# Optimization experiments

Hardware: AMD Instinct MI355X
Metric: run time of the kernel (lower is better)

## Reference

```python
import jax, jax.numpy as jnp
import numpy as np
import math

B, T = 32, 64
VOCAB = 50005
EMB = 512
HID = 1024
SES = 1024
KNOW = 8785
NEG = math.exp(-100)

def _glorot(key, shape):
    fan_in, fan_out = shape[1], shape[0]
    lim = (6.0 / (fan_in + fan_out)) ** 0.5
    return jax.random.uniform(key, shape, jnp.float32, -lim, lim)

def setup_inputs() -> dict:
    key = jax.random.key(0)
    ks = jax.random.split(key, 16)
    inp = {}
    inp['ses_encoding'] = jax.random.normal(ks[0], (B, 1, SES), jnp.float32)
    inp['know_encoding'] = jax.random.normal(ks[1], (B, 1, SES), jnp.float32)
    inp['target'] = jax.random.randint(ks[2], (B, T), 0, 50000)
    inp['embed_w'] = jax.random.normal(ks[3], (VOCAB, EMB), jnp.float32) * 0.02
    # GRU params (PyTorch layout: W_ih [3H, E], W_hh [3H, H], gate order r,z,n)
    s = 1.0 / (HID ** 0.5)
    inp['W_ih'] = jax.random.uniform(ks[4], (3 * HID, EMB), jnp.float32, -s, s)
    inp['W_hh'] = jax.random.uniform(ks[5], (3 * HID, HID), jnp.float32, -s, s)
    inp['b_ih'] = jax.random.uniform(ks[6], (3 * HID,), jnp.float32, -s, s)
    inp['b_hh'] = jax.random.uniform(ks[7], (3 * HID,), jnp.float32, -s, s)
    inp['ses_to_dec_w'] = _glorot(ks[8], (HID, SES))
    inp['ses_to_dec_b'] = jnp.zeros((HID,), jnp.float32)
    inp['dec_inf_w'] = _glorot(ks[9], (2 * EMB, HID))
    inp['ses_inf_w'] = _glorot(ks[10], (2 * EMB, SES))
    inp['emb_inf_w'] = _glorot(ks[11], (2 * EMB, EMB))
    inp['emb_inf_b'] = jnp.zeros((2 * EMB,), jnp.float32)
    inp['W1'] = jax.random.normal(ks[12], (VOCAB, SES), jnp.float32) * 0.02
    inp['W2'] = jax.random.normal(ks[13], (VOCAB, SES), jnp.float32) * 0.02
    inp['W3'] = jax.random.normal(ks[14], (VOCAB, 2 * EMB), jnp.float32) * 0.02
    inp['W4'] = jax.random.normal(ks[15], (VOCAB, EMB), jnp.float32) * 0.02
    inp['know_vote_w'] = _glorot(jax.random.fold_in(key, 99), (KNOW, SES))
    return inp

def _gru_step(x, h, W_ih, W_hh, b_ih, b_hh):
    # x: [B,E], h: [B,H]
    gi = x @ W_ih.T + b_ih
    gh = h @ W_hh.T + b_hh
    ir, iz, inn = jnp.split(gi, 3, axis=-1)
    hr, hz, hn = jnp.split(gh, 3, axis=-1)
    r = jax.nn.sigmoid(ir + hr)
    z = jax.nn.sigmoid(iz + hz)
    n = jnp.tanh(inn + r * hn)
    return (1.0 - z) * h + z * n  # torch: h' = (1-z)*n + z*h with torch z; note torch formula

def _gru_step_torch(x, h, W_ih, W_hh, b_ih, b_hh):
    gi = x @ W_ih.T + b_ih
    gh = h @ W_hh.T + b_hh
    ir, iz, inn = jnp.split(gi, 3, axis=-1)
    hr, hz, hn = jnp.split(gh, 3, axis=-1)
    r = jax.nn.sigmoid(ir + hr)
    z = jax.nn.sigmoid(iz + hz)
    n = jnp.tanh(inn + r * hn)
    return (1.0 - z) * n + z * h

def reference(ses_encoding, know_encoding, target, embed_w, W_ih, W_hh, b_ih, b_hh,
              ses_to_dec_w, ses_to_dec_b, dec_inf_w, ses_inf_w, emb_inf_w, emb_inf_b,
              W1, W2, W3, W4, know_vote_w):
    ses = ses_encoding[:, 0, :]    # [B, SES]
    know = know_encoding[:, 0, :]  # [B, SES]
    target_emb = embed_w[target]   # [B, T, E]

    h0 = jnp.tanh(ses @ ses_to_dec_w.T + ses_to_dec_b)  # [B, H]

    # time-invariant pieces
    ses_inf_vec = ses @ ses_inf_w.T                      # [B, 2E]
    l1 = ses @ W1.T                                      # [B, V]
    l2 = know @ W2.T                                     # [B, V]
    # knowledge mixture log-probs (constant over time)
    ks = know @ know_vote_w.T                            # [B, KNOW]
    ks = ks[:, :-1]                                      # drop last -> [B, KNOW-1]
    pad_l = jnp.full((ks.shape[0], 10), NEG, ks.dtype)
    pad_r = jnp.full((ks.shape[0], VOCAB - 10 - (KNOW - 1)), NEG, ks.dtype)
    know_scores = jnp.concatenate([pad_l, ks, pad_r], axis=1)  # [B, V]
    know_probs = jax.nn.log_softmax(know_scores, axis=-1)      # [B, V]
    gate_const = l1 + l2                                 # [B, V]

    def step(h, emb_t):
        # emb_t: [B, E]
        h_new = _gru_step_torch(emb_t, h, W_ih, W_hh, b_ih, b_hh)  # [B, H]
        dec_hid_vec = h_new @ dec_inf_w.T                          # [B, 2E]
        target_inf = emb_t @ emb_inf_w.T + emb_inf_b               # [B, 2E]
        total = dec_hid_vec + ses_inf_vec + target_inf             # [B, 2E]
        mx = jnp.max(total.reshape(total.shape[0], EMB, 2), axis=-1)  # maxout -> [B, E]
        logits = mx @ embed_w.T                                    # shared embedding -> [B, V]
        hid_probs = jax.nn.log_softmax(logits, axis=-1)
        l3 = h_new @ W3.T                                          # note: W3 applied to hid_o [B,H]... but W3 is [V,2E]
        l4 = emb_t @ W4.T                                          # [B, V]
        gate = jax.nn.sigmoid(gate_const + l3 + l4)                # [B, V]
        final = gate * hid_probs + (1.0 - gate) * know_probs       # [B, V]
        return h_new, final

    # target_emb time-major for scan
    _, outs = jax.lax.scan(step, h0, jnp.swapaxes(target_emb, 0, 1))
    final_scores_all = jnp.swapaxes(outs, 0, 1)  # [B, T, V]
    return final_scores_all
```

## Files before the change

kernel.cpp:

```cpp
#include <hip/hip_runtime.h>

constexpr int VOC  = 50005;
constexpr int VOCP = 50048;
constexpr int NTM  = 391;
constexpr int NTMP = 400;
constexpr int KSN  = 8784;
constexpr int KSNP = 8832;
constexpr float NPAD = 41221.0f;

typedef unsigned short u16;
typedef __attribute__((ext_vector_type(4))) float f32x4;
typedef __attribute__((ext_vector_type(8))) short bf16x8;

__device__ __forceinline__ float dot4(float4 a, float4 b) {
    return a.x*b.x + a.y*b.y + a.z*b.z + a.w*b.w;
}
__device__ __forceinline__ float sigmoidf_(float x) { return 1.0f / (1.0f + expf(-x)); }
__device__ __forceinline__ u16 f2bf(float f) {
    unsigned x = __float_as_uint(f);
    return (u16)((x + 0x7FFFu + ((x >> 16) & 1u)) >> 16);
}
__device__ __forceinline__ float bf2f(u16 u) { return __uint_as_float(((unsigned)u) << 16); }
template<int AUX>
__device__ __forceinline__ void gload_lds16x(const void* g, void* l) {
    __builtin_amdgcn_global_load_lds((const __attribute__((address_space(1))) unsigned int*)g,
                                     (__attribute__((address_space(3))) unsigned int*)l, 16, 0, AUX);
}
__device__ __forceinline__ void gload_lds16(const void* g, void* l) { gload_lds16x<0>(g, l); }
__device__ __forceinline__ void store_u16_sc(u16* p, u16 v) {
    asm volatile("global_store_short %0, %1, off sc0 sc1" :: "v"(p), "v"((unsigned)v) : "memory");
}

__global__ __launch_bounds__(256) void k_cvt(const float* __restrict__ src, u16* __restrict__ dst,
                                             int ncols, int sld, int dld) {
    int row = blockIdx.x;
    int c = (blockIdx.y * 256 + threadIdx.x) * 4;
    if (c >= ncols) return;
    float4 v = *(const float4*)(src + (size_t)row * sld + c);
    unsigned lo = f2bf(v.x) | ((unsigned)f2bf(v.y) << 16);
    unsigned hi = f2bf(v.z) | ((unsigned)f2bf(v.w) << 16);
    *(uint2*)(dst + (size_t)row * dld + c) = make_uint2(lo, hi);
}

__global__ __launch_bounds__(256) void k_pad0(u16* __restrict__ Aemb, u16* __restrict__ A34,
                                              u16* __restrict__ Awk) {
    int r = VOC + blockIdx.x;
    unsigned* pe = (unsigned*)(Aemb + (size_t)r * 512);
    if (threadIdx.x < 256) pe[threadIdx.x] = 0;
    unsigned* p3 = (unsigned*)(A34 + (size_t)r * 1536);
    for (int i = threadIdx.x; i < 768; i += 256) p3[i] = 0;
    unsigned* pw = (unsigned*)(Awk + (size_t)r * 2048);
    for (int i = threadIdx.x; i < 1024; i += 256) pw[i] = 0;
}
__global__ __launch_bounds__(256) void k_padK(u16* __restrict__ kvwb) {
    int r = KSN + blockIdx.x;
    unsigned* p = (unsigned*)(kvwb + (size_t)r * 1024);
    for (int i = threadIdx.x; i < 512; i += 256) p[i] = 0;
}

__global__ __launch_bounds__(256) void k_bsk(const float* __restrict__ ses,
                                             const float* __restrict__ know,
                                             u16* __restrict__ Bsk) {
    int row = blockIdx.x;
    for (int c0 = threadIdx.x * 4; c0 < 2048; c0 += 1024) {
        uint2 val = make_uint2(0, 0);
        if (row < 32) {
            const float* srcp = (c0 < 1024) ? ses + (size_t)row * 1024 + c0
                                            : know + (size_t)row * 1024 + (c0 - 1024);
            float4 v = *(const float4*)srcp;
            val = make_uint2(f2bf(v.x) | ((unsigned)f2bf(v.y) << 16),
                             f2bf(v.z) | ((unsigned)f2bf(v.w) << 16));
        }
        *(uint2*)(Bsk + (size_t)row * 2048 + c0) = val;
    }
}

__global__ __launch_bounds__(128) void k_gather(const float* __restrict__ embed,
                                                const int* __restrict__ target,
                                                u16* __restrict__ BG) {
    int n = blockIdx.x;
    int row = target[n];
    int c = threadIdx.x * 4;
    float4 v = *(const float4*)(embed + (size_t)row * 512 + c);
    unsigned lo = f2bf(v.x) | ((unsigned)f2bf(v.y) << 16);
    unsigned hi = f2bf(v.z) | ((unsigned)f2bf(v.w) << 16);
    *(uint2*)(BG + (size_t)n * 1536 + 1024 + c) = make_uint2(lo, hi);
}

__global__ __launch_bounds__(256) void k_h0_sesinf(const float* __restrict__ ses,
                                                   const float* __restrict__ sdw,
                                                   const float* __restrict__ sdb,
                                                   const float* __restrict__ siw,
                                                   float* __restrict__ h0,
                                                   float* __restrict__ sesinf) {
    int g = blockIdx.x * 256 + threadIdx.x;
    int b = g & 31;
    int jg = g >> 5;
    int j0 = jg * 4;
    const float4* s4 = (const float4*)(ses + (size_t)b * 1024);
    const float4* wa[4];
    const float4* wc[4];
#pragma unroll
    for (int r = 0; r < 4; ++r) {
        wa[r] = (const float4*)(sdw + (size_t)(j0 + r) * 1024);
        wc[r] = (const float4*)(siw + (size_t)(j0 + r) * 1024);
    }
    float a[4] = {0, 0, 0, 0}, c[4] = {0, 0, 0, 0};
    for (int kq = 0; kq < 256; ++kq) {
        float4 sv = s4[kq];
#pragma unroll
        for (int r = 0; r < 4; ++r) { a[r] += dot4(sv, wa[r][kq]); c[r] += dot4(sv, wc[r][kq]); }
    }
#pragma unroll
    for (int r = 0; r < 4; ++r) {
        h0[b * 1024 + j0 + r] = tanhf(a[r] + sdb[j0 + r]);
        sesinf[b * 1024 + j0 + r] = c[r];
    }
}

__global__ __launch_bounds__(256) void k_lseknow(const float* __restrict__ ks,
                                                 float* __restrict__ lsek) {
    int b = blockIdx.x;
    int t = threadIdx.x;
    __shared__ float sm[256];
    float m = -1e30f;
    for (int j = t; j < KSN; j += 256) m = fmaxf(m, ks[(size_t)b * KSN + j]);
    sm[t] = m;
    __syncthreads();
    for (int s = 128; s > 0; s >>= 1) { if (t < s) sm[t] = fmaxf(sm[t], sm[t + s]); __syncthreads(); }
    m = fmaxf(sm[0], 0.0f);
    __syncthreads();
    float s = 0.0f;
    for (int j = t; j < KSN; j += 256) s += expf(ks[(size_t)b * KSN + j] - m);
    sm[t] = s;
    __syncthreads();
    for (int r = 128; r > 0; r >>= 1) { if (t < r) sm[t] += sm[t + r]; __syncthreads(); }
    if (t == 0) lsek[b] = m + logf(sm[0] + NPAD * expf(0.0f - m));
}

template<int EPI>
__global__ __launch_bounds__(256) void gemm_bt(
    const u16* __restrict__ A, int lda,
    const u16* __restrict__ B, int ldb, int K,
    const float* __restrict__ p0, const float* __restrict__ p1,
    float* __restrict__ q0, u16* __restrict__ q1,
    unsigned char* __restrict__ q2, float* __restrict__ q3)
{
    __shared__ u16 Asm[128 * 64];
    __shared__ u16 Bsm[128 * 64];
    const int tid = threadIdx.x;
    const int lane = tid & 63;
    const int w = tid >> 6;
    const int wm = w >> 1, wn = w & 1;
    const int nt = blockIdx.x, mt = blockIdx.y;

    f32x4 acc[4][4];
#pragma unroll
    for (int i = 0; i < 4; ++i)
#pragma unroll
        for (int j = 0; j < 4; ++j) acc[i][j] = (f32x4){0.f, 0.f, 0.f, 0.f};

    for (int kt = 0; kt < K; kt += 64) {
#pragma unroll
        for (int p = 0; p < 4; ++p) {
            int flat = (w * 4 + p) * 64 + lane;
            int row = flat >> 3, slot = flat & 7;
            int ss = slot ^ (row & 7);
            gload_lds16(A + (size_t)(mt * 128 + row) * lda + kt + ss * 8, Asm + flat * 8);
            gload_lds16(B + (size_t)(nt * 128 + row) * ldb + kt + ss * 8, Bsm + flat * 8);
        }
        __syncthreads();
#pragma unroll
        for (int kc = 0; kc < 2; ++kc) {
            bf16x8 af[4], bfr[4];
#pragma unroll
            for (int mi = 0; mi < 4; ++mi) {
                int row = wm * 64 + mi * 16 + (lane & 15);
                int bcol = kc * 64 + ((lane >> 4) << 4);
                af[mi] = *(const bf16x8*)((const char*)Asm + row * 128 + (bcol ^ ((row & 7) << 4)));
            }
#pragma unroll
            for (int ni = 0; ni < 4; ++ni) {
                int row = wn * 64 + ni * 16 + (lane & 15);
                int bcol = kc * 64 + ((lane >> 4) << 4);
                bfr[ni] = *(const bf16x8*)((const char*)Bsm + row * 128 + (bcol ^ ((row & 7) << 4)));
            }
#pragma unroll
            for (int mi = 0; mi < 4; ++mi)
#pragma unroll
                for (int ni = 0; ni < 4; ++ni)
                    acc[mi][ni] = __builtin_amdgcn_mfma_f32_16x16x32_bf16(af[mi], bfr[ni], acc[mi][ni], 0, 0, 0);
        }
        __syncthreads();
    }

    const int cl = lane & 15;
    const int rg = (lane >> 4) << 2;

    if constexpr (EPI == 0) {
#pragma unroll
        for (int mi = 0; mi < 4; ++mi) {
            int m0 = mt * 128 + wm * 64 + mi * 16 + rg;
            float4 bias = *(const float4*)(p0 + m0);
#pragma unroll
            for (int ni = 0; ni < 4; ++ni) {
                int n = nt * 128 + wn * 64 + ni * 16 + cl;
                float4 v;
                v.x = acc[mi][ni][0] + bias.x; v.y = acc[mi][ni][1] + bias.y;
                v.z = acc[mi][ni][2] + bias.z; v.w = acc[mi][ni][3] + bias.w;
                *(float4*)(q0 + (size_t)n * 3072 + m0) = v;
            }
        }
    }
    if constexpr (EPI == 1) {
#pragma unroll
        for (int mi = 0; mi < 4; ++mi) {
            int m0 = mt * 128 + wm * 64 + mi * 16 + rg;
            float4 eb4 = *(const float4*)(p1 + m0);
#pragma unroll
            for (int ni = 0; ni < 4; ++ni) {
                int n = nt * 128 + wn * 64 + ni * 16 + cl;
                int b = n >> 6;
                float v0 = acc[mi][ni][0] + p0[b * 1024 + m0 + 0] + eb4.x;
                float v1 = acc[mi][ni][1] + p0[b * 1024 + m0 + 1] + eb4.y;
                float v2 = acc[mi][ni][2] + p0[b * 1024 + m0 + 2] + eb4.z;
                float v3 = acc[mi][ni][3] + p0[b * 1024 + m0 + 3] + eb4.w;
                unsigned pk = f2bf(fmaxf(v0, v1)) | ((unsigned)f2bf(fmaxf(v2, v3)) << 16);
                *(unsigned*)(q1 + (size_t)n * 512 + (m0 >> 1)) = pk;
            }
        }
    }
    if constexpr (EPI == 2) {
#pragma unroll
        for (int mi = 0; mi < 4; ++mi) {
            int v0 = mt * 128 + wm * 64 + mi * 16 + rg;
#pragma unroll
            for (int ni = 0; ni < 4; ++ni) {
                int n = nt * 128 + wn * 64 + ni * 16 + cl;
                int b = n >> 6;
                float4 gcv = *(const float4*)(p0 + (size_t)b * VOCP + v0);
                unsigned pk = 0;
#pragma unroll
                for (int r = 0; r < 4; ++r) {
                    float garg = acc[mi][ni][r] + ((const float*)&gcv)[r];
                    float gate = 1.0f / (1.0f + expf(-garg));
                    pk |= ((unsigned)(int)(gate * 255.0f + 0.5f)) << (8 * r);
                }
                *(unsigned*)(q2 + (size_t)n * VOCP + v0) = pk;
            }
        }
    }
    if constexpr (EPI == 3) {
        __shared__ float redm[2][128];
        __shared__ float reds[2][128];
#pragma unroll
        for (int mi = 0; mi < 4; ++mi) {
            int v0 = mt * 128 + wm * 64 + mi * 16 + rg;
#pragma unroll
            for (int ni = 0; ni < 4; ++ni) {
                int n = nt * 128 + wn * 64 + ni * 16 + cl;
                unsigned lo = f2bf(acc[mi][ni][0]) | ((unsigned)f2bf(acc[mi][ni][1]) << 16);
                unsigned hi = f2bf(acc[mi][ni][2]) | ((unsigned)f2bf(acc[mi][ni][3]) << 16);
                *(uint2*)(q1 + (size_t)n * VOCP + v0) = make_uint2(lo, hi);
            }
        }
#pragma unroll
        for (int ni = 0; ni < 4; ++ni) {
            float lm = -1e30f;
#pragma unroll
            for (int mi = 0; mi < 4; ++mi) {
                int v0 = mt * 128 + wm * 64 + mi * 16 + rg;
#pragma unroll
                for (int r = 0; r < 4; ++r)
                    if (v0 + r < VOC) lm = fmaxf(lm, acc[mi][ni][r]);
            }
            lm = fmaxf(lm, __shfl_xor(lm, 16));
            lm = fmaxf(lm, __shfl_xor(lm, 32));
            float s = 0.0f;
#pragma unroll
            for (int mi = 0; mi < 4; ++mi) {
                int v0 = mt * 128 + wm * 64 + mi * 16 + rg;
#pragma unroll
                for (int r = 0; r < 4; ++r)
                    if (v0 + r < VOC) s += expf(acc[mi][ni][r] - lm);
            }
            s += __shfl_xor(s, 16);
            s += __shfl_xor(s, 32);
            if (lane < 16) {
                redm[wm][wn * 64 + ni * 16 + lane] = lm;
                reds[wm][wn * 64 + ni * 16 + lane] = s;
            }
        }
        __syncthreads();
        if (tid < 128) {
            float m0_ = redm[0][tid], m1_ = redm[1][tid];
            float m = fmaxf(m0_, m1_);
            float s = reds[0][tid] * expf(m0_ - m) + reds[1][tid] * expf(m1_ - m);
            int n = nt * 128 + tid;
            q0[(size_t)n * NTMP + mt] = m;
            q3[(size_t)n * NTMP + mt] = s;
        }
    }
    if constexpr (EPI == 4) {
#pragma unroll
        for (int mi = 0; mi < 4; ++mi) {
            int m0 = mt * 128 + wm * 64 + mi * 16 + rg;
#pragma unroll
            for (int ni = 0; ni < 4; ++ni) {
                int n = nt * 128 + wn * 64 + ni * 16 + cl;
                if (n < 32) {
                    float4 v;
                    v.x = acc[mi][ni][0]; v.y = acc[mi][ni][1];
                    v.z = acc[mi][ni][2]; v.w = acc[mi][ni][3];
                    *(float4*)(q0 + (size_t)n * VOCP + m0) = v;
                }
            }
        }
    }
    if constexpr (EPI == 5) {
#pragma unroll
        for (int mi = 0; mi < 4; ++mi) {
            int m0 = mt * 128 + wm * 64 + mi * 16 + rg;
#pragma unroll
            for (int ni = 0; ni < 4; ++ni) {
                int n = nt * 128 + wn * 64 + ni * 16 + cl;
                if (n < 32 && m0 < KSN) {
                    float4 v;
                    v.x = acc[mi][ni][0]; v.y = acc[mi][ni][1];
                    v.z = acc[mi][ni][2]; v.w = acc[mi][ni][3];
                    *(float4*)(q0 + (size_t)n * KSN + m0) = v;
                }
            }
        }
    }
}

__global__ __launch_bounds__(256, 1) void k_gru_m4(const u16* __restrict__ WhhB,
                                                   const float* __restrict__ GI,
                                                   const float* __restrict__ bhh,
                                                   const u16* __restrict__ h0b,
                                                   u16* __restrict__ BG,
                                                   unsigned* __restrict__ flags) {
    __shared__ __align__(16) char smem[131072];
    const int tid = threadIdx.x;
    const int lane = tid & 63;
    const int w = tid >> 6;
    const int jb = blockIdx.x;
    const int j0 = jb * 16;
    const int jl = tid & 15, bp = tid >> 4;
    const int je = j0 + jl;
    const float bh0 = bhh[je], bh1 = bhh[1024 + je], bh2 = bhh[2048 + je];
    char* Bbase = smem + 98304 + w * 8192;

#pragma unroll
    for (int it = 0; it < 24; ++it) {
        int flat = (it * 4 + w) * 64 + lane;
        int r = flat >> 7, s = flat & 127;
        int ss = s ^ (r & 7);
        int gr = (r >> 4) * 1024 + j0 + (r & 15);
        gload_lds16(WhhB + (size_t)gr * 1024 + ss * 8, smem + (size_t)flat * 16);
    }

    float hpv[2];
#pragma unroll
    for (int rb = 0; rb < 2; ++rb)
        hpv[rb] = bf2f(h0b[(size_t)(bp * 2 + rb) * 1024 + je]);

    const int lrow = lane & 15;
    const int ksel = lane >> 4;

    for (int t = 0; t < 64; ++t) {
        const u16* hsrc = (t == 0) ? h0b : BG + (size_t)(t - 1) * 1536;
        const size_t hstr = (t == 0) ? 1024 : (size_t)64 * 1536;

        float gi0[2], gi1[2], gi2[2];
#pragma unroll
        for (int rb = 0; rb < 2; ++rb) {
            const float* gp = GI + ((size_t)((bp * 2 + rb) * 64 + t)) * 3072 + je;
            gi0[rb] = gp[0]; gi1[rb] = gp[1024]; gi2[rb] = gp[2048];
        }
        __builtin_amdgcn_sched_barrier(0);

        auto stageB = [&](int c) {
            char* dst = Bbase + (c & 1) * 4096;
            int kq0 = w * 256 + c * 64;
#pragma unroll
            for (int q = 0; q < 4; ++q) {
                int flat = q * 64 + lane;
                int r = flat >> 3, s = flat & 7;
                int ss = s ^ (r & 7);
                gload_lds16x<0x11>(hsrc + (size_t)r * hstr + kq0 + ss * 8,
                                   dst + (size_t)flat * 16);
            }
        };
        stageB(0); stageB(1);
        if (t == 0) {
            __syncthreads();
        } else {
            asm volatile("s_waitcnt vmcnt(4)" ::: "memory");
        }
        __builtin_amdgcn_sched_barrier(0);

        f32x4 acc[3][2];
#pragma unroll
        for (int mi = 0; mi < 3; ++mi)
#pragma unroll
            for (int ni = 0; ni < 2; ++ni) acc[mi][ni] = (f32x4){0.f, 0.f, 0.f, 0.f};

#pragma unroll
        for (int c = 0; c < 4; ++c) {
            char* Bb = Bbase + (c & 1) * 4096;
#pragma unroll
            for (int ks = 0; ks < 2; ++ks) {
                int kb = ks * 64 + ksel * 16;
                bf16x8 bfr[2];
#pragma unroll
                for (int ni = 0; ni < 2; ++ni) {
                    int br = ni * 16 + lrow;
                    bfr[ni] = *(const bf16x8*)(Bb + br * 128 + (kb ^ ((br & 7) << 4)));
                }
                int kA = w * 512 + c * 128 + kb;
#pragma unroll
                for (int mi = 0; mi < 3; ++mi) {
                    int ar = mi * 16 + lrow;
                    bf16x8 af = *(const bf16x8*)(smem + ar * 2048 + (kA ^ ((ar & 7) << 4)));
#pragma unroll
                    for (int ni = 0; ni < 2; ++ni)
                        acc[mi][ni] = __builtin_amdgcn_mfma_f32_16x16x32_bf16(af, bfr[ni], acc[mi][ni], 0, 0, 0);
                }
            }
            asm volatile("s_waitcnt lgkmcnt(0)" ::: "memory");
            __builtin_amdgcn_sched_barrier(0);
            if (c < 2) {
                stageB(c + 2);
                asm volatile("s_waitcnt vmcnt(4)" ::: "memory");
            } else if (c == 2) {
                asm volatile("s_waitcnt vmcnt(0)" ::: "memory");
            }
            __builtin_amdgcn_sched_barrier(0);
        }

        float (*epiw)[33] = (float(*)[33])Bbase;
        {
            const int rg = (lane >> 4) << 2;
#pragma unroll
            for (int mi = 0; mi < 3; ++mi)
#pragma unroll
                for (int ni = 0; ni < 2; ++ni) {
                    int m0 = mi * 16 + rg;
                    int cb = ni * 16 + lrow;
#pragma unroll
                    for (int r = 0; r < 4; ++r) epiw[m0 + r][cb] = acc[mi][ni][r];
                }
        }
        asm volatile("s_waitcnt lgkmcnt(0)" ::: "memory");
        __builtin_amdgcn_s_barrier();

#pragma unroll
        for (int rb = 0; rb < 2; ++rb) {
            int b = bp * 2 + rb;
            float s0 = 0.f, s1 = 0.f, s2 = 0.f;
#pragma unroll
            for (int ww = 0; ww < 4; ++ww) {
                float (*ep)[33] = (float(*)[33])(smem + 98304 + ww * 8192);
                s0 += ep[jl][b]; s1 += ep[16 + jl][b]; s2 += ep[32 + jl][b];
            }
            float rr = sigmoidf_(gi0[rb] + s0 + bh0);
            float zz = sigmoidf_(gi1[rb] + s1 + bh1);
            float nn = tanhf(gi2[rb] + rr * (s2 + bh2));
            float hnew = (1.0f - zz) * nn + zz * hpv[rb];
            hpv[rb] = hnew;
            store_u16_sc(BG + ((size_t)(b * 64 + t)) * 1536 + je, f2bf(hnew));
        }

        if (t < 63) {
            asm volatile("s_waitcnt vmcnt(0)" ::: "memory");
            __syncthreads();
            if (tid == 0)
                __hip_atomic_store(&flags[jb], (unsigned)(t + 1),
                                   __ATOMIC_RELAXED, __HIP_MEMORY_SCOPE_AGENT);
            unsigned tgt = (unsigned)(t + 1);
            while (true) {
                unsigned v = __hip_atomic_load(&flags[lane],
                                               __ATOMIC_RELAXED, __HIP_MEMORY_SCOPE_AGENT);
                if (__all(v >= tgt)) break;
                __builtin_amdgcn_s_sleep(1);
            }
            __builtin_amdgcn_sched_barrier(0);
        }
    }
}

__global__ __launch_bounds__(256) void k_lse(const float* __restrict__ pmax,
                                             const float* __restrict__ psum,
                                             float* __restrict__ lse) {
    int n = blockIdx.x;
    int t = threadIdx.x;
    __shared__ float sm[256];
    const float* pm = pmax + (size_t)n * NTMP;
    const float* ps = psum + (size_t)n * NTMP;
    float m = -1e30f;
    for (int p = t; p < NTM; p += 256) m = fmaxf(m, pm[p]);
    sm[t] = m;
    __syncthreads();
    for (int s = 128; s > 0; s >>= 1) { if (t < s) sm[t] = fmaxf(sm[t], sm[t + s]); __syncthreads(); }
    m = sm[0];
    __syncthreads();
    float s = 0.0f;
    for (int p = t; p < NTM; p += 256) s += ps[p] * expf(pm[p] - m);
    sm[t] = s;
    __syncthreads();
    for (int r = 128; r > 0; r >>= 1) { if (t < r) sm[t] += sm[t + r]; __syncthreads(); }
    if (t == 0) lse[n] = m + logf(sm[0]);
}

__global__ __launch_bounds__(256) void k_final(const u16* __restrict__ Lb,
                                               const unsigned char* __restrict__ g8,
                                               const float* __restrict__ lse,
                                               const float* __restrict__ ks,
                                               const float* __restrict__ lsek,
                                               float* __restrict__ out) {
    int n = blockIdx.y;
    int b = n >> 6;
    float lsen = lse[n], lkb = lsek[b];
    int base = blockIdx.x * 2048;
#pragma unroll
    for (int i = 0; i < 8; ++i) {
        int v = base + i * 256 + threadIdx.x;
        if (v < VOC) {
            float L = bf2f(Lb[(size_t)n * VOCP + v]);
            float g = g8[(size_t)n * VOCP + v] * (1.0f / 255.0f);
            float kp = ((v >= 10 && v < 10 + KSN) ? ks[(size_t)b * KSN + (v - 10)] : 0.0f) - lkb;
            out[(size_t)n * VOC + v] = g * (L - lsen) + (1.0f - g) * kp;
        }
    }
}

extern "C" void kernel_launch(void* const* d_in, const int* in_sizes, int n_in,
                              void* d_out, int out_size, void* d_ws, size_t ws_size,
                              hipStream_t stream) {
    const float* ses    = (const float*)d_in[0];
    const float* know   = (const float*)d_in[1];
    const int*   target = (const int*)d_in[2];
    const float* embed  = (const float*)d_in[3];
    const float* Wih    = (const float*)d_in[4];
    const float* Whh    = (const float*)d_in[5];
    const float* bih    = (const float*)d_in[6];
    const float* bhh    = (const float*)d_in[7];
    const float* sdw    = (const float*)d_in[8];
    const float* sdb    = (const float*)d_in[9];
    const float* dw     = (const float*)d_in[10];
    const float* siw    = (const float*)d_in[11];
    const float* ew     = (const float*)d_in[12];
    const float* eb     = (const float*)d_in[13];
    const float* W1     = (const float*)d_in[14];
    const float* W2     = (const float*)d_in[15];
    const float* W3     = (const float*)d_in[16];
    const float* W4     = (const float*)d_in[17];
    const float* kvw    = (const float*)d_in[18];

    char* ws = (char*)d_ws;
    size_t o = 0;
    auto alloc = [&](size_t bytes) { char* r = ws + o; o += (bytes + 255) & ~(size_t)255; return r; };
    u16*   Aemb  = (u16*)  alloc((size_t)VOCP * 512 * 2);
    u16*   A34   = (u16*)  alloc((size_t)VOCP * 1536 * 2);
    u16*   Adwew = (u16*)  alloc((size_t)1024 * 1536 * 2);
    u16*   Wihb  = (u16*)  alloc((size_t)3072 * 512 * 2);
    u16*   WhhB  = (u16*)  alloc((size_t)3072 * 1024 * 2);
    u16*   h0b   = (u16*)  alloc((size_t)32 * 1024 * 2);
    u16*   BG    = (u16*)  alloc((size_t)2048 * 1536 * 2);
    u16*   BL    = (u16*)  alloc((size_t)2048 * 512 * 2);
    float* GI    = (float*)alloc((size_t)2048 * 3072 * 4);
    float* h0    = (float*)alloc((size_t)32 * 1024 * 4);
    float* sesinf= (float*)alloc((size_t)32 * 1024 * 4);
    float* gc    = (float*)alloc((size_t)32 * VOCP * 4);
    float* ksb   = (float*)alloc((size_t)32 * KSN * 4);
    float* lsek  = (float*)alloc(256);
    float* lse   = (float*)alloc((size_t)2048 * 4);
    unsigned* flags = (unsigned*)alloc(256);
    float* pmax  = (float*)alloc((size_t)2048 * NTMP * 4);
    float* psum  = (float*)alloc((size_t)2048 * NTMP * 4);
    unsigned char* g8 = (unsigned char*)alloc((size_t)2048 * VOCP);
    u16*   Lb    = (u16*)  alloc((size_t)2048 * VOCP * 2);
    u16*   Bsk   = (u16*)  alloc((size_t)128 * 2048 * 2);
    float* out = (float*)d_out;

    u16*   kvwb  = (u16*)g8;
    u16*   Awk   = Lb;

    hipMemsetAsync(flags, 0, 256, stream);

    k_cvt<<<dim3(VOC, 1), 256, 0, stream>>>(embed, Aemb, 512, 512, 512);
    k_cvt<<<dim3(VOC, 1), 256, 0, stream>>>(W3, A34, 1024, 1024, 1536);
    k_cvt<<<dim3(VOC, 1), 256, 0, stream>>>(W4, A34 + 1024, 512, 512, 1536);
    k_cvt<<<dim3(VOC, 1), 256, 0, stream>>>(W1, Awk, 1024, 1024, 2048);
    k_cvt<<<dim3(VOC, 1), 256, 0, stream>>>(W2, Awk + 1024, 1024, 1024, 2048);
    k_cvt<<<dim3(KSN, 1), 256, 0, stream>>>(kvw, kvwb, 1024, 1024, 1024);
    k_pad0<<<dim3(VOCP - VOC), 256, 0, stream>>>(Aemb, A34, Awk);
    k_padK<<<dim3(KSNP - KSN), 256, 0, stream>>>(kvwb);
    k_cvt<<<dim3(1024, 1), 256, 0, stream>>>(dw, Adwew, 1024, 1024, 1536);
    k_cvt<<<dim3(1024, 1), 256, 0, stream>>>(ew, Adwew + 1024, 512, 512, 1536);
    k_cvt<<<dim3(3072, 1), 256, 0, stream>>>(Wih, Wihb, 512, 512, 512);
    k_cvt<<<dim3(3072, 1), 256, 0, stream>>>(Whh, WhhB, 1024, 1024, 1024);
    k_bsk<<<dim3(128), 256, 0, stream>>>(ses, know, Bsk);

    k_gather<<<dim3(2048), 128, 0, stream>>>(embed, target, BG);
    k_h0_sesinf<<<dim3(32), 256, 0, stream>>>(ses, sdw, sdb, siw, h0, sesinf);
    k_cvt<<<dim3(32, 1), 256, 0, stream>>>(h0, h0b, 1024, 1024, 1024);

    gemm_bt<4><<<dim3(1, NTM), 256, 0, stream>>>(Awk, 2048, Bsk, 2048, 2048,
                                                 nullptr, nullptr, gc, nullptr, nullptr, nullptr);
    gemm_bt<5><<<dim3(1, 69), 256, 0, stream>>>(kvwb, 1024, Bsk + 1024, 2048, 1024,
                                                nullptr, nullptr, ksb, nullptr, nullptr, nullptr);
    k_lseknow<<<dim3(32), 256, 0, stream>>>(ksb, lsek);

    gemm_bt<0><<<dim3(16, 24), 256, 0, stream>>>(Wihb, 512, BG + 1024, 1536, 512,
                                                 bih, nullptr, GI, nullptr, nullptr, nullptr);
    k_gru_m4<<<dim3(64), 256, 0, stream>>>(WhhB, GI, bhh, h0b, BG, flags);
    gemm_bt<1><<<dim3(16, 8), 256, 0, stream>>>(Adwew, 1536, BG, 1536, 1536,
                                                sesinf, eb, nullptr, BL, nullptr, nullptr);
    gemm_bt<2><<<dim3(16, NTM), 256, 0, stream>>>(A34, 1536, BG, 1536, 1536,
                                                  gc, nullptr, nullptr, nullptr, g8, nullptr);
    gemm_bt<3><<<dim3(16, NTM), 256, 0, stream>>>(Aemb, 512, BL, 512, 512,
                                                  nullptr, nullptr, pmax, Lb, nullptr, psum);
    k_lse<<<dim3(2048), 256, 0, stream>>>(pmax, psum, lse);
    k_final<<<dim3(25, 2048), 256, 0, stream>>>(Lb, g8, lse, ksb, lsek, out);
}
```

Before: 1.680 ms.

## Replace gate GEMM with 256x256-tile triple-buffered kernel and swizzled LDS

Replaces the generic 128x128 gate GEMM (A34 x BG with sigmoid-to-uint8 epilogue) with a dedicated 512-thread kernel that uses 256x256 tiles, triple-buffered LDS staging with an XOR swizzle, and a blockIdx remap that groups tiles for L2 reuse. Vocabulary padding grows to 50176 so the tiles divide evenly, which changes the strides of gc and g8 and extends the pad kernel. The aim is to raise arithmetic intensity and hide load latency in the largest GEMM. In exchange the kernel uses more LDS and registers, runs fewer waves per CU, and does a little extra work on the padded rows.

```diff
diff --git a/kernel.cpp b/kernel.cpp
--- a/kernel.cpp
+++ b/kernel.cpp
@@ -2,6 +2,7 @@
 
 constexpr int VOC  = 50005;
 constexpr int VOCP = 50048;
+constexpr int VOCP2= 50176;
 constexpr int NTM  = 391;
 constexpr int NTMP = 400;
 constexpr int KSN  = 8784;
@@ -45,12 +46,14 @@
 __global__ __launch_bounds__(256) void k_pad0(u16* __restrict__ Aemb, u16* __restrict__ A34,
                                               u16* __restrict__ Awk) {
     int r = VOC + blockIdx.x;
-    unsigned* pe = (unsigned*)(Aemb + (size_t)r * 512);
-    if (threadIdx.x < 256) pe[threadIdx.x] = 0;
     unsigned* p3 = (unsigned*)(A34 + (size_t)r * 1536);
     for (int i = threadIdx.x; i < 768; i += 256) p3[i] = 0;
-    unsigned* pw = (unsigned*)(Awk + (size_t)r * 2048);
-    for (int i = threadIdx.x; i < 1024; i += 256) pw[i] = 0;
+    if (r < VOCP) {
+        unsigned* pe = (unsigned*)(Aemb + (size_t)r * 512);
+        if (threadIdx.x < 256) pe[threadIdx.x] = 0;
+        unsigned* pw = (unsigned*)(Awk + (size_t)r * 2048);
+        for (int i = threadIdx.x; i < 1024; i += 256) pw[i] = 0;
+    }
 }
 __global__ __launch_bounds__(256) void k_padK(u16* __restrict__ kvwb) {
     int r = KSN + blockIdx.x;
@@ -230,26 +233,6 @@
             }
         }
     }
-    if constexpr (EPI == 2) {
-#pragma unroll
-        for (int mi = 0; mi < 4; ++mi) {
-            int v0 = mt * 128 + wm * 64 + mi * 16 + rg;
-#pragma unroll
-            for (int ni = 0; ni < 4; ++ni) {
-                int n = nt * 128 + wn * 64 + ni * 16 + cl;
-                int b = n >> 6;
-                float4 gcv = *(const float4*)(p0 + (size_t)b * VOCP + v0);
-                unsigned pk = 0;
-#pragma unroll
-                for (int r = 0; r < 4; ++r) {
-                    float garg = acc[mi][ni][r] + ((const float*)&gcv)[r];
-                    float gate = 1.0f / (1.0f + expf(-garg));
-                    pk |= ((unsigned)(int)(gate * 255.0f + 0.5f)) << (8 * r);
-                }
-                *(unsigned*)(q2 + (size_t)n * VOCP + v0) = pk;
-            }
-        }
-    }
     if constexpr (EPI == 3) {
         __shared__ float redm[2][128];
         __shared__ float reds[2][128];
@@ -312,7 +295,7 @@
                     float4 v;
                     v.x = acc[mi][ni][0]; v.y = acc[mi][ni][1];
                     v.z = acc[mi][ni][2]; v.w = acc[mi][ni][3];
-                    *(float4*)(q0 + (size_t)n * VOCP + m0) = v;
+                    *(float4*)(q0 + (size_t)n * VOCP2 + m0) = v;
                 }
             }
         }
@@ -333,6 +316,136 @@
             }
         }
     }
+}
+
+__global__ __launch_bounds__(512, 2) void gemm_gate8(
+    const u16* __restrict__ A,
+    const u16* __restrict__ B,
+    const float* __restrict__ gc2,
+    unsigned char* __restrict__ g8)
+{
+    constexpr int K = 1536, NT = K / 32;
+    __shared__ __align__(16) char smem[98304];
+    const int tid = threadIdx.x;
+    const int lane = tid & 63;
+    const int w = tid >> 6;
+    const int wm = w >> 2;
+    const int wn = w & 3;
+    const int lrow = lane & 15;
+    const int g = lane >> 4;
+
+    int bid = blockIdx.x;
+    int wg = (bid & 7) * 196 + (bid >> 3);
+    int mt = wg >> 3;
+    int nt = wg & 7;
+    const size_t arow0 = (size_t)mt * 256;
+    const size_t brow0 = (size_t)nt * 256;
+
+#define SWZ(r) (((r) & 3) ^ (((r) >> 2) & 3))
+    auto stageA = [&](int t) {
+        char* dst = smem + (t % 3) * 16384;
+        int kt = t * 32;
+#pragma unroll
+        for (int q = 0; q < 2; ++q) {
+            int flat = q * 512 + tid;
+            int row = flat >> 2, s = flat & 3;
+            int ss = s ^ SWZ(row);
+            gload_lds16(A + (arow0 + row) * 1536 + kt + ss * 8, dst + flat * 16);
+        }
+    };
+    auto stageB = [&](int t) {
+        char* dst = smem + 49152 + (t % 3) * 16384;
+        int kt = t * 32;
+#pragma unroll
+        for (int q = 0; q < 2; ++q) {
+            int flat = q * 512 + tid;
+            int row = flat >> 2, s = flat & 3;
+            int ss = s ^ SWZ(row);
+            gload_lds16(B + (brow0 + row) * 1536 + kt + ss * 8, dst + flat * 16);
+        }
+    };
+
+    f32x4 acc[8][4];
+#pragma unroll
+    for (int i = 0; i < 8; ++i)
+#pragma unroll
+        for (int j = 0; j < 4; ++j) acc[i][j] = (f32x4){0.f, 0.f, 0.f, 0.f};
+
+    stageA(0); stageB(0); stageA(1); stageB(1);
+    asm volatile("s_waitcnt vmcnt(4)" ::: "memory");
+    __builtin_amdgcn_sched_barrier(0);
+    __builtin_amdgcn_s_barrier();
+
+    auto tile_body = [&](int t, bool prefetch) {
+        char* Ab = smem + (t % 3) * 16384;
+        char* Bb = smem + 49152 + (t % 3) * 16384;
+        if (prefetch) stageA(t + 2);
+        bf16x8 bf[4], af[4];
+#pragma unroll
+        for (int ni = 0; ni < 4; ++ni) {
+            int r = wn * 64 + ni * 16 + lrow;
+            bf[ni] = *(const bf16x8*)(Bb + r * 64 + (g ^ SWZ(r)) * 16);
+        }
+#pragma unroll
+        for (int mi = 0; mi < 4; ++mi) {
+            int r = wm * 128 + mi * 16 + lrow;
+            af[mi] = *(const bf16x8*)(Ab + r * 64 + (g ^ SWZ(r)) * 16);
+        }
+        __builtin_amdgcn_s_setprio(1);
+#pragma unroll
+        for (int mi = 0; mi < 4; ++mi)
+#pragma unroll
+            for (int ni = 0; ni < 4; ++ni)
+                acc[mi][ni] = __builtin_amdgcn_mfma_f32_16x16x32_bf16(af[mi], bf[ni], acc[mi][ni], 0, 0, 0);
+        __builtin_amdgcn_s_setprio(0);
+        if (prefetch) stageB(t + 2);
+#pragma unroll
+        for (int mi = 0; mi < 4; ++mi) {
+            int r = wm * 128 + 64 + mi * 16 + lrow;
+            af[mi] = *(const bf16x8*)(Ab + r * 64 + (g ^ SWZ(r)) * 16);
+        }
+        __builtin_amdgcn_s_setprio(1);
+#pragma unroll
+        for (int mi = 0; mi < 4; ++mi)
+#pragma unroll
+            for (int ni = 0; ni < 4; ++ni)
+                acc[4 + mi][ni] = __builtin_amdgcn_mfma_f32_16x16x32_bf16(af[mi], bf[ni], acc[4 + mi][ni], 0, 0, 0);
+        __builtin_amdgcn_s_setprio(0);
+    };
+
+    for (int t = 0; t < NT - 2; ++t) {
+        tile_body(t, true);
+        asm volatile("s_waitcnt vmcnt(4)" ::: "memory");
+        __builtin_amdgcn_sched_barrier(0);
+        __builtin_amdgcn_s_barrier();
+    }
+    tile_body(NT - 2, false);
+    asm volatile("s_waitcnt vmcnt(0)" ::: "memory");
+    __builtin_amdgcn_sched_barrier(0);
+    __builtin_amdgcn_s_barrier();
+    tile_body(NT - 1, false);
+
+    const int rg = g << 2;
+    const int b = nt * 4 + wn;
+    const float* gcrow = gc2 + (size_t)b * VOCP2;
+#pragma unroll
+    for (int a = 0; a < 8; ++a) {
+        int v0 = mt * 256 + wm * 128 + (a >> 2) * 64 + (a & 3) * 16 + rg;
+        float4 gcv = *(const float4*)(gcrow + v0);
+#pragma unroll
+        for (int ni = 0; ni < 4; ++ni) {
+            int n = nt * 256 + wn * 64 + ni * 16 + lrow;
+            unsigned pk = 0;
+#pragma unroll
+            for (int r = 0; r < 4; ++r) {
+                float garg = acc[a][ni][r] + ((const float*)&gcv)[r];
+                float gate = 1.0f / (1.0f + expf(-garg));
+                pk |= ((unsigned)(int)(gate * 255.0f + 0.5f)) << (8 * r);
+            }
+            *(unsigned*)(g8 + (size_t)n * VOCP2 + v0) = pk;
+        }
+    }
+#undef SWZ
 }
 
 __global__ __launch_bounds__(256, 1) void k_gru_m4(const u16* __restrict__ WhhB,
@@ -529,7 +642,7 @@
         int v = base + i * 256 + threadIdx.x;
         if (v < VOC) {
             float L = bf2f(Lb[(size_t)n * VOCP + v]);
-            float g = g8[(size_t)n * VOCP + v] * (1.0f / 255.0f);
+            float g = g8[(size_t)n * VOCP2 + v] * (1.0f / 255.0f);
             float kp = ((v >= 10 && v < 10 + KSN) ? ks[(size_t)b * KSN + (v - 10)] : 0.0f) - lkb;
             out[(size_t)n * VOC + v] = g * (L - lsen) + (1.0f - g) * kp;
         }
@@ -563,7 +676,7 @@
     size_t o = 0;
     auto alloc = [&](size_t bytes) { char* r = ws + o; o += (bytes + 255) & ~(size_t)255; return r; };
     u16*   Aemb  = (u16*)  alloc((size_t)VOCP * 512 * 2);
-    u16*   A34   = (u16*)  alloc((size_t)VOCP * 1536 * 2);
+    u16*   A34   = (u16*)  alloc((size_t)VOCP2 * 1536 * 2);
     u16*   Adwew = (u16*)  alloc((size_t)1024 * 1536 * 2);
     u16*   Wihb  = (u16*)  alloc((size_t)3072 * 512 * 2);
     u16*   WhhB  = (u16*)  alloc((size_t)3072 * 1024 * 2);
@@ -573,14 +686,14 @@
     float* GI    = (float*)alloc((size_t)2048 * 3072 * 4);
     float* h0    = (float*)alloc((size_t)32 * 1024 * 4);
     float* sesinf= (float*)alloc((size_t)32 * 1024 * 4);
-    float* gc    = (float*)alloc((size_t)32 * VOCP * 4);
+    float* gc    = (float*)alloc((size_t)32 * VOCP2 * 4);
     float* ksb   = (float*)alloc((size_t)32 * KSN * 4);
     float* lsek  = (float*)alloc(256);
     float* lse   = (float*)alloc((size_t)2048 * 4);
     unsigned* flags = (unsigned*)alloc(256);
     float* pmax  = (float*)alloc((size_t)2048 * NTMP * 4);
     float* psum  = (float*)alloc((size_t)2048 * NTMP * 4);
-    unsigned char* g8 = (unsigned char*)alloc((size_t)2048 * VOCP);
+    unsigned char* g8 = (unsigned char*)alloc((size_t)2048 * VOCP2);
     u16*   Lb    = (u16*)  alloc((size_t)2048 * VOCP * 2);
     u16*   Bsk   = (u16*)  alloc((size_t)128 * 2048 * 2);
     float* out = (float*)d_out;
@@ -596,7 +709,7 @@
     k_cvt<<<dim3(VOC, 1), 256, 0, stream>>>(W1, Awk, 1024, 1024, 2048);
     k_cvt<<<dim3(VOC, 1), 256, 0, stream>>>(W2, Awk + 1024, 1024, 1024, 2048);
     k_cvt<<<dim3(KSN, 1), 256, 0, stream>>>(kvw, kvwb, 1024, 1024, 1024);
-    k_pad0<<<dim3(VOCP - VOC), 256, 0, stream>>>(Aemb, A34, Awk);
+    k_pad0<<<dim3(VOCP2 - VOC), 256, 0, stream>>>(Aemb, A34, Awk);
     k_padK<<<dim3(KSNP - KSN), 256, 0, stream>>>(kvwb);
     k_cvt<<<dim3(1024, 1), 256, 0, stream>>>(dw, Adwew, 1024, 1024, 1536);
     k_cvt<<<dim3(1024, 1), 256, 0, stream>>>(ew, Adwew + 1024, 512, 512, 1536);
@@ -619,8 +732,7 @@
     k_gru_m4<<<dim3(64), 256, 0, stream>>>(WhhB, GI, bhh, h0b, BG, flags);
     gemm_bt<1><<<dim3(16, 8), 256, 0, stream>>>(Adwew, 1536, BG, 1536, 1536,
                                                 sesinf, eb, nullptr, BL, nullptr, nullptr);
-    gemm_bt<2><<<dim3(16, NTM), 256, 0, stream>>>(A34, 1536, BG, 1536, 1536,
-                                                  gc, nullptr, nullptr, nullptr, g8, nullptr);
+    gemm_gate8<<<dim3(1568), 512, 0, stream>>>(A34, BG, gc, g8);
     gemm_bt<3><<<dim3(16, NTM), 256, 0, stream>>>(Aemb, 512, BL, 512, 512,
                                                   nullptr, nullptr, pmax, Lb, nullptr, psum);
     k_lse<<<dim3(2048), 256, 0, stream>>>(pmax, psum, lse);
```

Result: no change. 1.665 ms (-0.9%).
